# Kernel optimization log

Hardware: AMD Instinct MI355X
Metric: run time of the kernel (lower is better)

## Reference

```python
import jax, jax.numpy as jnp
import numpy as np

B, I, O, DEG = 16384, 1024, 1024, 8

def setup_inputs() -> dict:
    key = jax.random.key(0)
    kx, kc = jax.random.split(key)
    x = jax.random.normal(kx, (B, I), dtype=jnp.float32)
    std = 1.0 / (I * (DEG + 1))
    cheby_coeffs = jax.random.normal(kc, (I, O, DEG + 1), dtype=jnp.float32) * std
    return {"x": x, "cheby_coeffs": cheby_coeffs}


def reference(x, cheby_coeffs):
    # Chebyshev basis: T_d(tanh(x)) = cos(d * acos(tanh(x)))
    deg = cheby_coeffs.shape[-1]
    arange = jnp.arange(deg, dtype=x.dtype)  # (D+1,)
    theta = jnp.arccos(jnp.tanh(x))          # (B, I)
    basis = jnp.cos(theta[:, :, None] * arange)  # (B, I, D+1)
    y = jnp.einsum('bid,iod->bo', basis, cheby_coeffs)
    return y
```

## Files before the change

### kernel.cpp

```cpp
#include <hip/hip_runtime.h>
#include <hip/hip_bf16.h>


#define WSCALE 4096.0f
#define INV_WSCALE (1.0f/4096.0f)

typedef _Float16 f16;
typedef __fp16   hf2  __attribute__((ext_vector_type(2)));
typedef _Float16 f16x8 __attribute__((ext_vector_type(8)));
typedef float    f32x4 __attribute__((ext_vector_type(4)));
typedef float    f32x16 __attribute__((ext_vector_type(16)));

union F16x8u { hf2 h2[4]; f16x8 v8; };

__global__ __launch_bounds__(256) void wt_transform(const float* __restrict__ cc,
                                                    f16* __restrict__ wt) {
  int t    = blockIdx.x * 256 + threadIdx.x;
  int j4   = t & 127;
  int grp  = t >> 7;
  int ncol = grp & 7;
  int rest = grp >> 3;
  int ic   = rest & 31;
  int d    = rest >> 5;
  int u    = j4 >> 5;
  int h    = (j4 >> 4) & 1;
  int r    = j4 & 15;
  int rk   = (r >> 1) & 3;
  size_t base = (size_t)(d * 32 + ic) * 32768 + (size_t)ncol * 4096 + (size_t)j4 * 32;
#pragma unroll
  for (int v = 0; v < 4; ++v) {
    int tt = v ^ rk;
    int q  = tt & 1, kl = tt >> 1;
    int o  = ncol * 128 + u * 32 + q * 16 + r;
    int ib = ic * 32 + h * 16 + kl * 8;
    f16x8 val;
#pragma unroll
    for (int e = 0; e < 8; ++e)
      val[e] = (f16)(cc[((size_t)(ib + e) * 1024 + o) * 9 + d] * WSCALE);
    *(f16x8*)(wt + base + v * 8) = val;
  }
}

__global__ __launch_bounds__(256) void t2_transform(const float* __restrict__ x,
                                                    f16* __restrict__ t2) {
  size_t gid = (size_t)blockIdx.x * 256 + threadIdx.x;
  const float* p = x + gid * 8;
  f32x4 a = *(const f32x4*)p;
  f32x4 b = *(const f32x4*)(p + 4);
  float tf[8];
#pragma unroll
  for (int e = 0; e < 8; ++e) {
    float xx = (e < 4) ? a[e] : b[e - 4];
    tf[e] = 1.f - 2.f * __builtin_amdgcn_rcpf(__expf(2.f * xx) + 1.f);
  }
  F16x8u u;
#pragma unroll
  for (int q = 0; q < 4; ++q)
    u.h2[q] = __builtin_amdgcn_cvt_pkrtz(tf[2 * q], tf[2 * q + 1]);
  f16x8 v = u.v8 + u.v8;
  *(f16x8*)(t2 + gid * 8) = v;
}

__global__ __launch_bounds__(512, 2) void cheby_gemm(const f16* __restrict__ t2g,
                                                     const f16* __restrict__ wt,
                                                     float* __restrict__ out) {
  __shared__ f16 bbuf[18][4096];

  const int tid  = threadIdx.x;
  const int wid  = tid >> 6;
  const int lane = tid & 63;
  const int lr   = lane & 31;
  const int lh   = lane >> 5;
  const int wm   = wid >> 1;
  const int wn   = wid & 1;
  const int mrow = blockIdx.x >> 3;
  const int ncol = blockIdx.x & 7;
  const int m0   = mrow * 256 + wm * 64;
  const int n0   = ncol * 128 + wn * 64;
  const int rbase = wn * 2048 + ((lane & 15) * 4 + ((lane >> 4) ^ ((lane >> 1) & 3))) * 8;

  auto stage = [&](int cn, int dn, int buf) {
    const f16* src = wt + (size_t)(dn * 32 + cn) * 32768 + (size_t)ncol * 4096;
    __builtin_amdgcn_global_load_lds(
        (const __attribute__((address_space(1))) unsigned*)(src + tid * 8),
        (__attribute__((address_space(3))) unsigned*)(&bbuf[buf][wid * 512]),
        16, 0, 0);
  };

  f32x16 acc[2][2];
#pragma unroll
  for (int a = 0; a < 2; ++a)
#pragma unroll
    for (int b = 0; b < 2; ++b)
#pragma unroll
      for (int j = 0; j < 16; ++j) acc[a][b][j] = 0.f;

  const f16x8 ones  = {(f16)1,(f16)1,(f16)1,(f16)1,(f16)1,(f16)1,(f16)1,(f16)1};
  const f16x8 half8 = {(f16)0.5f,(f16)0.5f,(f16)0.5f,(f16)0.5f,
                       (f16)0.5f,(f16)0.5f,(f16)0.5f,(f16)0.5f};
  f16x8 t2v[2][2], t2n[2][2];

  auto loadx = [&](int cn) {
#pragma unroll
    for (int mb = 0; mb < 2; ++mb)
#pragma unroll
      for (int h = 0; h < 2; ++h)
        t2n[mb][h] = *(const f16x8*)(t2g + (size_t)(m0 + mb * 32 + lr) * 1024
                                         + cn * 32 + h * 16 + lh * 8);
  };

#define REC(NEW, S1, S2)                                                       \
  _Pragma("unroll") for (int mb = 0; mb < 2; ++mb)                             \
    _Pragma("unroll") for (int h = 0; h < 2; ++h)                              \
      NEW[mb][h] = __builtin_elementwise_fma(t2v[mb][h], S1[mb][h], -S2[mb][h]);

#define LOADB(BD, SB, DIDX)                                                    \
  {                                                                            \
    const f16* bb = &bbuf[0][0] + (SB) + (DIDX) * 4096 + rbase;                \
    BD[0][0] = *(const f16x8*)&bb[0];    BD[0][1] = *(const f16x8*)&bb[512];   \
    BD[1][0] = *(const f16x8*)&bb[1024]; BD[1][1] = *(const f16x8*)&bb[1536];  \
  }

#define MFMA8(AF, BD)                                                          \
  {                                                                            \
    __builtin_amdgcn_s_setprio(1);                                             \
    _Pragma("unroll") for (int nb = 0; nb < 2; ++nb)                           \
      _Pragma("unroll") for (int mb = 0; mb < 2; ++mb) {                       \
        acc[mb][nb] = __builtin_amdgcn_mfma_f32_32x32x16_f16(AF[mb][0], BD[nb][0], \
                                                             acc[mb][nb], 0, 0, 0); \
        acc[mb][nb] = __builtin_amdgcn_mfma_f32_32x32x16_f16(AF[mb][1], BD[nb][1], \
                                                             acc[mb][nb], 0, 0, 0); \
      }                                                                        \
    __builtin_amdgcn_s_setprio(0);                                             \
  }

#define VMB(N)                                                                 \
  asm volatile("s_waitcnt vmcnt(" #N ")" ::: "memory");                        \
  __builtin_amdgcn_s_barrier();

#pragma unroll
  for (int d = 0; d < 9; ++d) stage(0, d, d);
  loadx(0);

  f16x8 onesA[2][2];
#pragma unroll
  for (int mb = 0; mb < 2; ++mb)
#pragma unroll
    for (int h = 0; h < 2; ++h) onesA[mb][h] = ones;

  f16x8 bfA[2][2], bfB[2][2];
  f16x8 A1[2][2], A2[2][2], A3[2][2], A4[2][2], A5[2][2], A6[2][2], A7[2][2], A8[2][2];

  for (int c = 0; c < 31; ++c) {
    const int sbase = (c & 1) * 36864;
    const int nbase = (1 - (c & 1)) * 9;

    VMB(7)
    LOADB(bfA, sbase, 0)
#pragma unroll
    for (int mb = 0; mb < 2; ++mb)
#pragma unroll
      for (int h = 0; h < 2; ++h) {
        t2v[mb][h] = t2n[mb][h];
        A1[mb][h]  = t2v[mb][h] * half8;
      }
    stage(c + 1, 0, nbase + 0);
    loadx(c + 1);
    LOADB(bfB, sbase, 1)
    MFMA8(onesA, bfA)

    VMB(11) stage(c + 1, 1, nbase + 1); LOADB(bfA, sbase, 2) REC(A2, A1, onesA) MFMA8(A1, bfB)
    VMB(11) stage(c + 1, 2, nbase + 2); LOADB(bfB, sbase, 3) REC(A3, A2, A1)    MFMA8(A2, bfA)
    VMB(11) stage(c + 1, 3, nbase + 3); LOADB(bfA, sbase, 4) REC(A4, A3, A2)    MFMA8(A3, bfB)
    VMB(11) stage(c + 1, 4, nbase + 4); LOADB(bfB, sbase, 5) REC(A5, A4, A3)    MFMA8(A4, bfA)
    VMB(11) stage(c + 1, 5, nbase + 5); LOADB(bfA, sbase, 6) REC(A6, A5, A4)    MFMA8(A5, bfB)
    VMB(11) stage(c + 1, 6, nbase + 6); LOADB(bfB, sbase, 7) REC(A7, A6, A5)    MFMA8(A6, bfA)
    VMB(11) stage(c + 1, 7, nbase + 7); LOADB(bfA, sbase, 8) REC(A8, A7, A6)    MFMA8(A7, bfB)

    stage(c + 1, 8, nbase + 8);
    MFMA8(A8, bfA)
  }

  {
    const int sbase = 36864;
    asm volatile("s_waitcnt vmcnt(0)" ::: "memory");
    __builtin_amdgcn_s_barrier();
    LOADB(bfA, sbase, 0)
#pragma unroll
    for (int mb = 0; mb < 2; ++mb)
#pragma unroll
      for (int h = 0; h < 2; ++h) {
        t2v[mb][h] = t2n[mb][h];
        A1[mb][h]  = t2v[mb][h] * half8;
      }
    LOADB(bfB, sbase, 1)
    MFMA8(onesA, bfA)
    LOADB(bfA, sbase, 2) REC(A2, A1, onesA) MFMA8(A1, bfB)
    LOADB(bfB, sbase, 3) REC(A3, A2, A1)    MFMA8(A2, bfA)
    LOADB(bfA, sbase, 4) REC(A4, A3, A2)    MFMA8(A3, bfB)
    LOADB(bfB, sbase, 5) REC(A5, A4, A3)    MFMA8(A4, bfA)
    LOADB(bfA, sbase, 6) REC(A6, A5, A4)    MFMA8(A5, bfB)
    LOADB(bfB, sbase, 7) REC(A7, A6, A5)    MFMA8(A6, bfA)
    LOADB(bfA, sbase, 8) REC(A8, A7, A6)    MFMA8(A7, bfB)
    MFMA8(A8, bfA)
  }
#undef REC
#undef LOADB
#undef MFMA8
#undef VMB

#pragma unroll
  for (int mb = 0; mb < 2; ++mb)
#pragma unroll
    for (int nb = 0; nb < 2; ++nb)
#pragma unroll
      for (int j = 0; j < 16; ++j) {
        int row = m0 + mb * 32 + 4 * lh + (j & 3) + 8 * (j >> 2);
        int col = n0 + nb * 32 + lr;
        out[(size_t)row * 1024 + col] = acc[mb][nb][j] * INV_WSCALE;
      }
}

__global__ __launch_bounds__(512, 2) void cheby_gemm_fb(const float* __restrict__ x,
                                                        const f16* __restrict__ wt,
                                                        float* __restrict__ out) {
  __shared__ f16 bbuf[18][4096];
  const int tid  = threadIdx.x;
  const int wid  = tid >> 6;
  const int lane = tid & 63;
  const int lr   = lane & 31;
  const int lh   = lane >> 5;
  const int wm   = wid >> 1;
  const int wn   = wid & 1;
  const int mrow = blockIdx.x >> 3;
  const int ncol = blockIdx.x & 7;
  const int m0   = mrow * 256 + wm * 64;
  const int n0   = ncol * 128 + wn * 64;
  const int rbase = wn * 2048 + ((lane & 15) * 4 + ((lane >> 4) ^ ((lane >> 1) & 3))) * 8;

  auto stage = [&](int cn, int dn, int buf) {
    const f16* src = wt + (size_t)(dn * 32 + cn) * 32768 + (size_t)ncol * 4096;
    __builtin_amdgcn_global_load_lds(
        (const __attribute__((address_space(1))) unsigned*)(src + tid * 8),
        (__attribute__((address_space(3))) unsigned*)(&bbuf[buf][wid * 512]),
        16, 0, 0);
  };
  auto stage9 = [&](int cn, int b0) {
#pragma unroll
    for (int d = 0; d < 9; ++d) stage(cn, d, b0 + d);
  };

  f32x16 acc[2][2];
#pragma unroll
  for (int a = 0; a < 2; ++a)
#pragma unroll
    for (int b = 0; b < 2; ++b)
#pragma unroll
      for (int j = 0; j < 16; ++j) acc[a][b][j] = 0.f;

  const f16x8 ones  = {(f16)1,(f16)1,(f16)1,(f16)1,(f16)1,(f16)1,(f16)1,(f16)1};
  const f16x8 half8 = {(f16)0.5f,(f16)0.5f,(f16)0.5f,(f16)0.5f,
                       (f16)0.5f,(f16)0.5f,(f16)0.5f,(f16)0.5f};
  f16x8 t2v[2][2], t2n[2][2];
  f32x4 xf[2][2][2];

  auto loadx = [&](int cn) {
#pragma unroll
    for (int mb = 0; mb < 2; ++mb)
#pragma unroll
      for (int h = 0; h < 2; ++h) {
        const float* p = x + (size_t)(m0 + mb * 32 + lr) * 1024 + cn * 32 + h * 16 + lh * 8;
        xf[mb][h][0] = *(const f32x4*)p;
        xf[mb][h][1] = *(const f32x4*)(p + 4);
      }
  };
  auto dotanh = [&]() {
#pragma unroll
    for (int mb = 0; mb < 2; ++mb)
#pragma unroll
      for (int h = 0; h < 2; ++h) {
        float tf[8];
#pragma unroll
        for (int e = 0; e < 8; ++e) {
          float xx = (e < 4) ? xf[mb][h][0][e] : xf[mb][h][1][e - 4];
          tf[e] = 1.f - 2.f * __builtin_amdgcn_rcpf(__expf(2.f * xx) + 1.f);
        }
        F16x8u u;
#pragma unroll
        for (int q = 0; q < 4; ++q)
          u.h2[q] = __builtin_amdgcn_cvt_pkrtz(tf[2 * q], tf[2 * q + 1]);
        t2n[mb][h] = u.v8 + u.v8;
      }
  };

#define REC(NEW, S1, S2)                                                       \
  _Pragma("unroll") for (int mb = 0; mb < 2; ++mb)                             \
    _Pragma("unroll") for (int h = 0; h < 2; ++h)                              \
      NEW[mb][h] = __builtin_elementwise_fma(t2v[mb][h], S1[mb][h], -S2[mb][h]);
#define CLUSTER(AF, DIDX)                                                      \
  {                                                                            \
    const f16* bb = &bbuf[0][0] + sbase + (DIDX) * 4096 + rbase;               \
    f16x8 bf[2][2];                                                            \
    _Pragma("unroll") for (int nb = 0; nb < 2; ++nb)                           \
      _Pragma("unroll") for (int h = 0; h < 2; ++h)                            \
        bf[nb][h] = *(const f16x8*)&bb[nb * 1024 + h * 512];                   \
    _Pragma("unroll") for (int nb = 0; nb < 2; ++nb)                           \
      _Pragma("unroll") for (int mb = 0; mb < 2; ++mb) {                       \
        acc[mb][nb] = __builtin_amdgcn_mfma_f32_32x32x16_f16(AF[mb][0], bf[nb][0], \
                                                             acc[mb][nb], 0, 0, 0); \
        acc[mb][nb] = __builtin_amdgcn_mfma_f32_32x32x16_f16(AF[mb][1], bf[nb][1], \
                                                             acc[mb][nb], 0, 0, 0); \
      }                                                                        \
  }

  stage9(0, 0);
  loadx(0);
  dotanh();

  f16x8 onesA[2][2];
#pragma unroll
  for (int mb = 0; mb < 2; ++mb)
#pragma unroll
    for (int h = 0; h < 2; ++h) onesA[mb][h] = ones;

  for (int c = 0; c < 32; ++c) {
    const bool lastc = (c == 31);
    const int  sbase = (c & 1) * 36864;
    const int  nbase = (1 - (c & 1)) * 9;

    asm volatile("s_waitcnt vmcnt(8)" ::: "memory");
    __builtin_amdgcn_s_barrier();

    f16x8 A1[2][2], A2[2][2], A3[2][2], A4[2][2], A5[2][2], A6[2][2], A7[2][2], A8[2][2];
#pragma unroll
    for (int mb = 0; mb < 2; ++mb)
#pragma unroll
      for (int h = 0; h < 2; ++h) {
        t2v[mb][h] = t2n[mb][h];
        A1[mb][h]  = t2v[mb][h] * half8;
      }
    if (!lastc) { stage9(c + 1, nbase); loadx(c + 1); }

    CLUSTER(onesA, 0)
    CLUSTER(A1, 1)
    REC(A2, A1, onesA)  CLUSTER(A2, 2)
    REC(A3, A2, A1)     CLUSTER(A3, 3)
    REC(A4, A3, A2)     CLUSTER(A4, 4)
    REC(A5, A4, A3)     CLUSTER(A5, 5)
    REC(A6, A5, A4)     CLUSTER(A6, 6)
    REC(A7, A6, A5)     CLUSTER(A7, 7)
    REC(A8, A7, A6)     CLUSTER(A8, 8)
    if (!lastc) dotanh();
  }
#undef REC
#undef CLUSTER

#pragma unroll
  for (int mb = 0; mb < 2; ++mb)
#pragma unroll
    for (int nb = 0; nb < 2; ++nb)
#pragma unroll
      for (int j = 0; j < 16; ++j) {
        int row = m0 + mb * 32 + 4 * lh + (j & 3) + 8 * (j >> 2);
        int col = n0 + nb * 32 + lr;
        out[(size_t)row * 1024 + col] = acc[mb][nb][j] * INV_WSCALE;
      }
}

extern "C" void kernel_launch(void* const* d_in, const int* in_sizes, int n_in,
                              void* d_out, int out_size, void* d_ws, size_t ws_size,
                              hipStream_t stream) {
  const float* x  = (const float*)d_in[0];
  const float* cc = (const float*)d_in[1];
  f16*   wt  = (f16*)d_ws;
  f16*   t2  = (f16*)((char*)d_ws + 18874368);
  float* out = (float*)d_out;

  hipLaunchKernelGGL(wt_transform, dim3(1152), dim3(256), 0, stream, cc, wt);
  if (ws_size >= 52428800) {
    hipLaunchKernelGGL(t2_transform, dim3(8192), dim3(256), 0, stream, x, t2);
    hipLaunchKernelGGL(cheby_gemm, dim3(512), dim3(512), 0, stream, t2, wt, out);
  } else {
    hipLaunchKernelGGL(cheby_gemm_fb, dim3(512), dim3(512), 0, stream, x, wt, out);
  }
}
```

Measured before the change: 333.3 us.

## Replace double-buffered LDS stages with a ten-slot rotating ring buffer

Shrinks the shared weight staging buffer from two full sets of nine degree slices to a ten-slot ring. Next-chunk slices are written into slots freed right after their data is consumed. This cuts LDS use so two blocks can reside per CU, aiming to improve latency hiding. It adds dynamic slot index arithmetic and tighter write-after-read ordering that relies on the existing barriers.

```diff
diff --git a/kernel.cpp b/kernel.cpp
--- a/kernel.cpp
+++ b/kernel.cpp
@@ -64,7 +64,7 @@
 __global__ __launch_bounds__(512, 2) void cheby_gemm(const f16* __restrict__ t2g,
                                                      const f16* __restrict__ wt,
                                                      float* __restrict__ out) {
-  __shared__ f16 bbuf[18][4096];
+  __shared__ f16 bbuf[10][4096];
 
   const int tid  = threadIdx.x;
   const int wid  = tid >> 6;
@@ -79,11 +79,11 @@
   const int n0   = ncol * 128 + wn * 64;
   const int rbase = wn * 2048 + ((lane & 15) * 4 + ((lane >> 4) ^ ((lane >> 1) & 3))) * 8;
 
-  auto stage = [&](int cn, int dn, int buf) {
+  auto stage = [&](int cn, int dn, int slot) {
     const f16* src = wt + (size_t)(dn * 32 + cn) * 32768 + (size_t)ncol * 4096;
     __builtin_amdgcn_global_load_lds(
         (const __attribute__((address_space(1))) unsigned*)(src + tid * 8),
-        (__attribute__((address_space(3))) unsigned*)(&bbuf[buf][wid * 512]),
+        (__attribute__((address_space(3))) unsigned*)(&bbuf[slot][wid * 512]),
         16, 0, 0);
   };
 
@@ -114,9 +114,9 @@
     _Pragma("unroll") for (int h = 0; h < 2; ++h)                              \
       NEW[mb][h] = __builtin_elementwise_fma(t2v[mb][h], S1[mb][h], -S2[mb][h]);
 
-#define LOADB(BD, SB, DIDX)                                                    \
+#define LOADB(BD, SLOT)                                                        \
   {                                                                            \
-    const f16* bb = &bbuf[0][0] + (SB) + (DIDX) * 4096 + rbase;                \
+    const f16* bb = &bbuf[(SLOT)][0] + rbase;                                  \
     BD[0][0] = *(const f16x8*)&bb[0];    BD[0][1] = *(const f16x8*)&bb[512];   \
     BD[1][0] = *(const f16x8*)&bb[1024]; BD[1][1] = *(const f16x8*)&bb[1536];  \
   }
@@ -151,12 +151,21 @@
   f16x8 bfA[2][2], bfB[2][2];
   f16x8 A1[2][2], A2[2][2], A3[2][2], A4[2][2], A5[2][2], A6[2][2], A7[2][2], A8[2][2];
 
+  int s0 = 0;
   for (int c = 0; c < 31; ++c) {
-    const int sbase = (c & 1) * 36864;
-    const int nbase = (1 - (c & 1)) * 9;
+    const int q0 = s0;
+    const int q1 = (s0 + 1 > 9) ? s0 - 9 : s0 + 1;
+    const int q2 = (s0 + 2 > 9) ? s0 - 8 : s0 + 2;
+    const int q3 = (s0 + 3 > 9) ? s0 - 7 : s0 + 3;
+    const int q4 = (s0 + 4 > 9) ? s0 - 6 : s0 + 4;
+    const int q5 = (s0 + 5 > 9) ? s0 - 5 : s0 + 5;
+    const int q6 = (s0 + 6 > 9) ? s0 - 4 : s0 + 6;
+    const int q7 = (s0 + 7 > 9) ? s0 - 3 : s0 + 7;
+    const int q8 = (s0 + 8 > 9) ? s0 - 2 : s0 + 8;
+    const int q9 = (s0 + 9 > 9) ? s0 - 1 : s0 + 9;
 
     VMB(7)
-    LOADB(bfA, sbase, 0)
+    LOADB(bfA, q0)
 #pragma unroll
     for (int mb = 0; mb < 2; ++mb)
 #pragma unroll
@@ -164,28 +173,39 @@
         t2v[mb][h] = t2n[mb][h];
         A1[mb][h]  = t2v[mb][h] * half8;
       }
-    stage(c + 1, 0, nbase + 0);
+    stage(c + 1, 0, q9);
     loadx(c + 1);
-    LOADB(bfB, sbase, 1)
+    LOADB(bfB, q1)
     MFMA8(onesA, bfA)
 
-    VMB(11) stage(c + 1, 1, nbase + 1); LOADB(bfA, sbase, 2) REC(A2, A1, onesA) MFMA8(A1, bfB)
-    VMB(11) stage(c + 1, 2, nbase + 2); LOADB(bfB, sbase, 3) REC(A3, A2, A1)    MFMA8(A2, bfA)
-    VMB(11) stage(c + 1, 3, nbase + 3); LOADB(bfA, sbase, 4) REC(A4, A3, A2)    MFMA8(A3, bfB)
-    VMB(11) stage(c + 1, 4, nbase + 4); LOADB(bfB, sbase, 5) REC(A5, A4, A3)    MFMA8(A4, bfA)
-    VMB(11) stage(c + 1, 5, nbase + 5); LOADB(bfA, sbase, 6) REC(A6, A5, A4)    MFMA8(A5, bfB)
-    VMB(11) stage(c + 1, 6, nbase + 6); LOADB(bfB, sbase, 7) REC(A7, A6, A5)    MFMA8(A6, bfA)
-    VMB(11) stage(c + 1, 7, nbase + 7); LOADB(bfA, sbase, 8) REC(A8, A7, A6)    MFMA8(A7, bfB)
-
-    stage(c + 1, 8, nbase + 8);
+    VMB(11) stage(c + 1, 1, q0); LOADB(bfA, q2) REC(A2, A1, onesA) MFMA8(A1, bfB)
+    VMB(11) stage(c + 1, 2, q1); LOADB(bfB, q3) REC(A3, A2, A1)    MFMA8(A2, bfA)
+    VMB(11) stage(c + 1, 3, q2); LOADB(bfA, q4) REC(A4, A3, A2)    MFMA8(A3, bfB)
+    VMB(11) stage(c + 1, 4, q3); LOADB(bfB, q5) REC(A5, A4, A3)    MFMA8(A4, bfA)
+    VMB(11) stage(c + 1, 5, q4); LOADB(bfA, q6) REC(A6, A5, A4)    MFMA8(A5, bfB)
+    VMB(11) stage(c + 1, 6, q5); LOADB(bfB, q7) REC(A7, A6, A5)    MFMA8(A6, bfA)
+    VMB(11) stage(c + 1, 7, q6); LOADB(bfA, q8) REC(A8, A7, A6)    MFMA8(A7, bfB)
+
+    stage(c + 1, 8, q7);
     MFMA8(A8, bfA)
+
+    s0 = (s0 == 0) ? 9 : s0 - 1;
   }
 
   {
-    const int sbase = 36864;
+    const int q0 = s0;
+    const int q1 = (s0 + 1 > 9) ? s0 - 9 : s0 + 1;
+    const int q2 = (s0 + 2 > 9) ? s0 - 8 : s0 + 2;
+    const int q3 = (s0 + 3 > 9) ? s0 - 7 : s0 + 3;
+    const int q4 = (s0 + 4 > 9) ? s0 - 6 : s0 + 4;
+    const int q5 = (s0 + 5 > 9) ? s0 - 5 : s0 + 5;
+    const int q6 = (s0 + 6 > 9) ? s0 - 4 : s0 + 6;
+    const int q7 = (s0 + 7 > 9) ? s0 - 3 : s0 + 7;
+    const int q8 = (s0 + 8 > 9) ? s0 - 2 : s0 + 8;
+
     asm volatile("s_waitcnt vmcnt(0)" ::: "memory");
     __builtin_amdgcn_s_barrier();
-    LOADB(bfA, sbase, 0)
+    LOADB(bfA, q0)
 #pragma unroll
     for (int mb = 0; mb < 2; ++mb)
 #pragma unroll
@@ -193,15 +213,15 @@
         t2v[mb][h] = t2n[mb][h];
         A1[mb][h]  = t2v[mb][h] * half8;
       }
-    LOADB(bfB, sbase, 1)
+    LOADB(bfB, q1)
     MFMA8(onesA, bfA)
-    LOADB(bfA, sbase, 2) REC(A2, A1, onesA) MFMA8(A1, bfB)
-    LOADB(bfB, sbase, 3) REC(A3, A2, A1)    MFMA8(A2, bfA)
-    LOADB(bfA, sbase, 4) REC(A4, A3, A2)    MFMA8(A3, bfB)
-    LOADB(bfB, sbase, 5) REC(A5, A4, A3)    MFMA8(A4, bfA)
-    LOADB(bfA, sbase, 6) REC(A6, A5, A4)    MFMA8(A5, bfB)
-    LOADB(bfB, sbase, 7) REC(A7, A6, A5)    MFMA8(A6, bfA)
-    LOADB(bfA, sbase, 8) REC(A8, A7, A6)    MFMA8(A7, bfB)
+    LOADB(bfA, q2) REC(A2, A1, onesA) MFMA8(A1, bfB)
+    LOADB(bfB, q3) REC(A3, A2, A1)    MFMA8(A2, bfA)
+    LOADB(bfA, q4) REC(A4, A3, A2)    MFMA8(A3, bfB)
+    LOADB(bfB, q5) REC(A5, A4, A3)    MFMA8(A4, bfA)
+    LOADB(bfA, q6) REC(A6, A5, A4)    MFMA8(A5, bfB)
+    LOADB(bfB, q7) REC(A7, A6, A5)    MFMA8(A6, bfA)
+    LOADB(bfA, q8) REC(A8, A7, A6)    MFMA8(A7, bfB)
     MFMA8(A8, bfA)
   }
 #undef REC
```

New measurement: 334.3 us. No clear change (+0.3%).

## Halve GEMM block size and replace double-buffer with 5-slot rotating LDS ring

Applied to the files above, without the earlier changes.

Each block shrinks from 512 to 256 threads (128 rows), and the launch uses 1024 blocks with three blocks per CU as the occupancy target. The 18-slab double buffer (all 9 Chebyshev degrees for two chunks) becomes a 5-slot ring that streams one degree slab at a time, roughly one cycle ahead, with each thread issuing two async loads per stage. LDS use drops from about 147KB to 40KB so more blocks fit per CU and latency is hidden across blocks. The s_setprio hints are removed. In exchange each block reuses the B tile over fewer rows, and the shallower prefetch increases the number of waits.

```diff
diff --git a/kernel.cpp b/kernel.cpp
--- a/kernel.cpp
+++ b/kernel.cpp
@@ -61,10 +61,10 @@
   *(f16x8*)(t2 + gid * 8) = v;
 }
 
-__global__ __launch_bounds__(512, 2) void cheby_gemm(const f16* __restrict__ t2g,
+__global__ __launch_bounds__(256, 3) void cheby_gemm(const f16* __restrict__ t2g,
                                                      const f16* __restrict__ wt,
                                                      float* __restrict__ out) {
-  __shared__ f16 bbuf[18][4096];
+  __shared__ f16 bbuf[5][4096];
 
   const int tid  = threadIdx.x;
   const int wid  = tid >> 6;
@@ -75,15 +75,19 @@
   const int wn   = wid & 1;
   const int mrow = blockIdx.x >> 3;
   const int ncol = blockIdx.x & 7;
-  const int m0   = mrow * 256 + wm * 64;
+  const int m0   = mrow * 128 + wm * 64;
   const int n0   = ncol * 128 + wn * 64;
   const int rbase = wn * 2048 + ((lane & 15) * 4 + ((lane >> 4) ^ ((lane >> 1) & 3))) * 8;
 
-  auto stage = [&](int cn, int dn, int buf) {
+  auto stage = [&](int cn, int dn, int slot) {
     const f16* src = wt + (size_t)(dn * 32 + cn) * 32768 + (size_t)ncol * 4096;
     __builtin_amdgcn_global_load_lds(
         (const __attribute__((address_space(1))) unsigned*)(src + tid * 8),
-        (__attribute__((address_space(3))) unsigned*)(&bbuf[buf][wid * 512]),
+        (__attribute__((address_space(3))) unsigned*)(&bbuf[slot][wid * 512]),
+        16, 0, 0);
+    __builtin_amdgcn_global_load_lds(
+        (const __attribute__((address_space(1))) unsigned*)(src + 2048 + tid * 8),
+        (__attribute__((address_space(3))) unsigned*)(&bbuf[slot][wid * 512 + 2048]),
         16, 0, 0);
   };
 
@@ -114,16 +118,15 @@
     _Pragma("unroll") for (int h = 0; h < 2; ++h)                              \
       NEW[mb][h] = __builtin_elementwise_fma(t2v[mb][h], S1[mb][h], -S2[mb][h]);
 
-#define LOADB(BD, SB, DIDX)                                                    \
+#define LOADB(BD, SLOT)                                                        \
   {                                                                            \
-    const f16* bb = &bbuf[0][0] + (SB) + (DIDX) * 4096 + rbase;                \
+    const f16* bb = &bbuf[0][0] + (SLOT) * 4096 + rbase;                       \
     BD[0][0] = *(const f16x8*)&bb[0];    BD[0][1] = *(const f16x8*)&bb[512];   \
     BD[1][0] = *(const f16x8*)&bb[1024]; BD[1][1] = *(const f16x8*)&bb[1536];  \
   }
 
 #define MFMA8(AF, BD)                                                          \
   {                                                                            \
-    __builtin_amdgcn_s_setprio(1);                                             \
     _Pragma("unroll") for (int nb = 0; nb < 2; ++nb)                           \
       _Pragma("unroll") for (int mb = 0; mb < 2; ++mb) {                       \
         acc[mb][nb] = __builtin_amdgcn_mfma_f32_32x32x16_f16(AF[mb][0], BD[nb][0], \
@@ -131,16 +134,15 @@
         acc[mb][nb] = __builtin_amdgcn_mfma_f32_32x32x16_f16(AF[mb][1], BD[nb][1], \
                                                              acc[mb][nb], 0, 0, 0); \
       }                                                                        \
-    __builtin_amdgcn_s_setprio(0);                                             \
   }
 
 #define VMB(N)                                                                 \
   asm volatile("s_waitcnt vmcnt(" #N ")" ::: "memory");                        \
   __builtin_amdgcn_s_barrier();
 
-#pragma unroll
-  for (int d = 0; d < 9; ++d) stage(0, d, d);
   loadx(0);
+  int p0 = 0, p1 = 1, p2 = 2, p3 = 3, p4 = 4;
+  stage(0, 0, p0); stage(0, 1, p1); stage(0, 2, p2); stage(0, 3, p3);
 
   f16x8 onesA[2][2];
 #pragma unroll
@@ -152,11 +154,8 @@
   f16x8 A1[2][2], A2[2][2], A3[2][2], A4[2][2], A5[2][2], A6[2][2], A7[2][2], A8[2][2];
 
   for (int c = 0; c < 31; ++c) {
-    const int sbase = (c & 1) * 36864;
-    const int nbase = (1 - (c & 1)) * 9;
-
-    VMB(7)
-    LOADB(bfA, sbase, 0)
+    VMB(4)
+    LOADB(bfA, p0)
 #pragma unroll
     for (int mb = 0; mb < 2; ++mb)
 #pragma unroll
@@ -164,28 +163,27 @@
         t2v[mb][h] = t2n[mb][h];
         A1[mb][h]  = t2v[mb][h] * half8;
       }
-    stage(c + 1, 0, nbase + 0);
+    stage(c, 4, p4);
     loadx(c + 1);
-    LOADB(bfB, sbase, 1)
+    LOADB(bfB, p1)
     MFMA8(onesA, bfA)
 
-    VMB(11) stage(c + 1, 1, nbase + 1); LOADB(bfA, sbase, 2) REC(A2, A1, onesA) MFMA8(A1, bfB)
-    VMB(11) stage(c + 1, 2, nbase + 2); LOADB(bfB, sbase, 3) REC(A3, A2, A1)    MFMA8(A2, bfA)
-    VMB(11) stage(c + 1, 3, nbase + 3); LOADB(bfA, sbase, 4) REC(A4, A3, A2)    MFMA8(A3, bfB)
-    VMB(11) stage(c + 1, 4, nbase + 4); LOADB(bfB, sbase, 5) REC(A5, A4, A3)    MFMA8(A4, bfA)
-    VMB(11) stage(c + 1, 5, nbase + 5); LOADB(bfA, sbase, 6) REC(A6, A5, A4)    MFMA8(A5, bfB)
-    VMB(11) stage(c + 1, 6, nbase + 6); LOADB(bfB, sbase, 7) REC(A7, A6, A5)    MFMA8(A6, bfA)
-    VMB(11) stage(c + 1, 7, nbase + 7); LOADB(bfA, sbase, 8) REC(A8, A7, A6)    MFMA8(A7, bfB)
-
-    stage(c + 1, 8, nbase + 8);
+    VMB(8) stage(c, 5, p0); LOADB(bfA, p2) REC(A2, A1, onesA) MFMA8(A1, bfB)
+    VMB(8) stage(c, 6, p1); LOADB(bfB, p3) REC(A3, A2, A1)    MFMA8(A2, bfA)
+    VMB(8) stage(c, 7, p2); LOADB(bfA, p4) REC(A4, A3, A2)    MFMA8(A3, bfB)
+    VMB(4) stage(c, 8, p3); LOADB(bfB, p0) REC(A5, A4, A3)    MFMA8(A4, bfA)
+    VMB(4) stage(c + 1, 0, p4); LOADB(bfA, p1) REC(A6, A5, A4) MFMA8(A5, bfB)
+    VMB(4) stage(c + 1, 1, p0); LOADB(bfB, p2) REC(A7, A6, A5) MFMA8(A6, bfA)
+    VMB(4) stage(c + 1, 2, p1); LOADB(bfA, p3) REC(A8, A7, A6) MFMA8(A7, bfB)
+    stage(c + 1, 3, p2);
     MFMA8(A8, bfA)
+
+    int tmp = p4; p4 = p3; p3 = p2; p2 = p1; p1 = p0; p0 = tmp;
   }
 
   {
-    const int sbase = 36864;
-    asm volatile("s_waitcnt vmcnt(0)" ::: "memory");
-    __builtin_amdgcn_s_barrier();
-    LOADB(bfA, sbase, 0)
+    VMB(4)
+    LOADB(bfA, p0)
 #pragma unroll
     for (int mb = 0; mb < 2; ++mb)
 #pragma unroll
@@ -193,15 +191,17 @@
         t2v[mb][h] = t2n[mb][h];
         A1[mb][h]  = t2v[mb][h] * half8;
       }
-    LOADB(bfB, sbase, 1)
+    stage(31, 4, p4);
+    LOADB(bfB, p1)
     MFMA8(onesA, bfA)
-    LOADB(bfA, sbase, 2) REC(A2, A1, onesA) MFMA8(A1, bfB)
-    LOADB(bfB, sbase, 3) REC(A3, A2, A1)    MFMA8(A2, bfA)
-    LOADB(bfA, sbase, 4) REC(A4, A3, A2)    MFMA8(A3, bfB)
-    LOADB(bfB, sbase, 5) REC(A5, A4, A3)    MFMA8(A4, bfA)
-    LOADB(bfA, sbase, 6) REC(A6, A5, A4)    MFMA8(A5, bfB)
-    LOADB(bfB, sbase, 7) REC(A7, A6, A5)    MFMA8(A6, bfA)
-    LOADB(bfA, sbase, 8) REC(A8, A7, A6)    MFMA8(A7, bfB)
+
+    VMB(4) stage(31, 5, p0); LOADB(bfA, p2) REC(A2, A1, onesA) MFMA8(A1, bfB)
+    VMB(4) stage(31, 6, p1); LOADB(bfB, p3) REC(A3, A2, A1)    MFMA8(A2, bfA)
+    VMB(4) stage(31, 7, p2); LOADB(bfA, p4) REC(A4, A3, A2)    MFMA8(A3, bfB)
+    VMB(4) stage(31, 8, p3); LOADB(bfB, p0) REC(A5, A4, A3)    MFMA8(A4, bfA)
+    VMB(4) LOADB(bfA, p1) REC(A6, A5, A4) MFMA8(A5, bfB)
+    VMB(2) LOADB(bfB, p2) REC(A7, A6, A5) MFMA8(A6, bfA)
+    VMB(0) LOADB(bfA, p3) REC(A8, A7, A6) MFMA8(A7, bfB)
     MFMA8(A8, bfA)
   }
 #undef REC
@@ -379,7 +379,7 @@
   hipLaunchKernelGGL(wt_transform, dim3(1152), dim3(256), 0, stream, cc, wt);
   if (ws_size >= 52428800) {
     hipLaunchKernelGGL(t2_transform, dim3(8192), dim3(256), 0, stream, x, t2);
-    hipLaunchKernelGGL(cheby_gemm, dim3(512), dim3(512), 0, stream, t2, wt, out);
+    hipLaunchKernelGGL(cheby_gemm, dim3(1024), dim3(256), 0, stream, t2, wt, out);
   } else {
     hipLaunchKernelGGL(cheby_gemm_fb, dim3(512), dim3(512), 0, stream, x, wt, out);
   }
```

Result: no change. 331.7 us (-0.5%).
